# Kernel tuning notes

Hardware: AMD Instinct MI355X
Metric: run time of the kernel (lower is better)

## Reference

```python
import jax, jax.numpy as jnp
from jax import lax
import numpy as np

K, O, I, KS = 4, 128, 128, 5
B, H, W = 32, 64, 64
PAD = 2


def setup_inputs() -> dict:
    key = jax.random.key(0)
    ks = jax.random.split(key, 7)
    x = jax.random.normal(ks[0], (B, I, H, W), dtype=jnp.float32)
    weight = jax.random.normal(ks[1], (K, O, I, KS, KS), dtype=jnp.float32)  # matches torch.randn init
    bias = jax.random.normal(ks[2], (K, O), dtype=jnp.float32)
    # attention: 1x1 convs on a (B,C,1,1) pooled tensor == dense layers
    a1_w = jax.random.normal(ks[3], (I, I), dtype=jnp.float32) * (1.0 / np.sqrt(I))
    a1_b = jax.random.normal(ks[4], (I,), dtype=jnp.float32) * 0.01
    a2_w = jax.random.normal(ks[5], (K, I), dtype=jnp.float32) * (1.0 / np.sqrt(I))
    a2_b = jax.random.normal(ks[6], (K,), dtype=jnp.float32) * 0.01
    return {"x": x, "weight": weight, "bias": bias,
            "a1_w": a1_w, "a1_b": a1_b, "a2_w": a2_w, "a2_b": a2_b}


def reference(x, weight, bias, a1_w, a1_b, a2_w, a2_b):
    Bn = x.shape[0]
    Kn, On, In, kh, kw = weight.shape
    # attention branch: global avg pool -> 1x1 conv -> relu -> 1x1 conv -> softmax over K
    pooled = jnp.mean(x, axis=(2, 3))                       # (B, C)
    h = jax.nn.relu(pooled @ a1_w.T + a1_b)                 # (B, C)
    attn = jax.nn.softmax(h @ a2_w.T + a2_b, axis=1)        # (B, K)
    # K parallel convs fused as one conv with K*O output channels (same math)
    w = weight.reshape(Kn * On, In, kh, kw)
    out = lax.conv_general_dilated(
        x, w, window_strides=(1, 1), padding=((PAD, PAD), (PAD, PAD)),
        dimension_numbers=("NCHW", "OIHW", "NCHW"))        # (B, K*O, H, W)
    Ho, Wo = out.shape[2], out.shape[3]
    out = out.reshape(Bn, Kn, On, Ho, Wo) + bias[None, :, :, None, None]
    # per-sample softmax-weighted combination over the K branches
    return jnp.einsum("bk,bkohw->bohw", attn, out)
```

## Files before the change

### kernel.cpp

```cpp
#include <hip/hip_runtime.h>
#include <stdint.h>

#define BATCH 32
#define ICH 128
#define OCH 128
#define KBR 4
#define HH 64
#define WW 64
#define TAPS 25
#define XROWS 8
#define XCOLS 68
#define XCP 40
#define WROWP 40

typedef __bf16 bf16x8 __attribute__((ext_vector_type(8)));
typedef float f32x4 __attribute__((ext_vector_type(4)));

static __device__ __forceinline__ ushort f2bf(float f) {
    union { float f; uint32_t u; } v; v.f = f;
    uint32_t u = v.u;
    uint32_t r = (u + 0x7FFFu + ((u >> 16) & 1u)) >> 16;
    return (ushort)r;
}
static __device__ __forceinline__ float bf2f(ushort s) {
    union { uint32_t u; float f; } v; v.u = ((uint32_t)s) << 16;
    return v.f;
}

__global__ __launch_bounds__(256) void k_prep(const float* __restrict__ x,
                                              ushort* __restrict__ xT,
                                              float* __restrict__ partial) {
    int blk = blockIdx.x;
    int b = blk >> 6, y = blk & 63;
    __shared__ __align__(16) uint tile2[64][65];
    const float* src = x + ((size_t)b * ICH) * (HH * WW) + (size_t)y * WW;
    int tid = threadIdx.x;
#pragma unroll
    for (int j = 0; j < 4; ++j) {
        int p = tid + 256 * j;
        int i2 = p >> 4, xc = (p & 15) * 4;
        float4 v0 = *(const float4*)(src + (size_t)(2 * i2) * (HH * WW) + xc);
        float4 v1 = *(const float4*)(src + (size_t)(2 * i2 + 1) * (HH * WW) + xc);
        tile2[xc + 0][i2] = (uint)f2bf(v0.x) | ((uint)f2bf(v1.x) << 16);
        tile2[xc + 1][i2] = (uint)f2bf(v0.y) | ((uint)f2bf(v1.y) << 16);
        tile2[xc + 2][i2] = (uint)f2bf(v0.z) | ((uint)f2bf(v1.z) << 16);
        tile2[xc + 3][i2] = (uint)f2bf(v0.w) | ((uint)f2bf(v1.w) << 16);
    }
    __syncthreads();
    uint* dst = (uint*)(xT + (((size_t)b * HH + y) * WW) * ICH);
#pragma unroll
    for (int j = 0; j < 16; ++j) {
        int p2 = tid + 256 * j;
        int xc = p2 >> 6, i2 = p2 & 63;
        dst[p2] = tile2[xc][i2];
    }
    if (tid < 128) {
        int i2 = tid >> 1, half = tid & 1;
        float s = 0.f;
        for (int xc = 0; xc < 64; ++xc) {
            uint v = tile2[xc][i2];
            s += bf2f((ushort)(half ? (v >> 16) : (v & 0xFFFFu)));
        }
        partial[((size_t)b * HH + y) * ICH + tid] = s;
    }
}

__global__ __launch_bounds__(128) void k_attn(const float* __restrict__ partial,
                                              const float* __restrict__ a1_w,
                                              const float* __restrict__ a1_b,
                                              const float* __restrict__ a2_w,
                                              const float* __restrict__ a2_b,
                                              const float* __restrict__ bias,
                                              float* __restrict__ attn,
                                              float* __restrict__ bias_eff) {
    int b = blockIdx.x;
    int t = threadIdx.x;
    __shared__ float pl[128], hh[128], lg[4], at[4];
    {
        float s = 0.f;
        const float* p = partial + (size_t)b * 64 * 128 + t;
        for (int y = 0; y < 64; ++y) s += p[y * 128];
        pl[t] = s * (1.f / 4096.f);
    }
    __syncthreads();
    {
        float a = a1_b[t];
        const float* w1 = a1_w + t * 128;
        for (int i = 0; i < 128; ++i) a += pl[i] * w1[i];
        hh[t] = a > 0.f ? a : 0.f;
    }
    __syncthreads();
    if (t < 4) {
        float l = a2_b[t];
        const float* w2 = a2_w + t * 128;
        for (int i = 0; i < 128; ++i) l += hh[i] * w2[i];
        lg[t] = l;
    }
    __syncthreads();
    if (t == 0) {
        float m = fmaxf(fmaxf(lg[0], lg[1]), fmaxf(lg[2], lg[3]));
        float e0 = expf(lg[0] - m), e1 = expf(lg[1] - m);
        float e2 = expf(lg[2] - m), e3 = expf(lg[3] - m);
        float inv = 1.f / (e0 + e1 + e2 + e3);
        at[0] = e0 * inv; at[1] = e1 * inv; at[2] = e2 * inv; at[3] = e3 * inv;
        attn[b * 4 + 0] = at[0]; attn[b * 4 + 1] = at[1];
        attn[b * 4 + 2] = at[2]; attn[b * 4 + 3] = at[3];
    }
    __syncthreads();
    bias_eff[b * 128 + t] = at[0] * bias[0 * 128 + t] + at[1] * bias[1 * 128 + t] +
                            at[2] * bias[2 * 128 + t] + at[3] * bias[3 * 128 + t];
}

__global__ __launch_bounds__(256) void k_wcomb(const float* __restrict__ weight,
                                               const float* __restrict__ attn,
                                               ushort* __restrict__ Weff) {
    int blk = blockIdx.x;
    int b = blk >> 7, o = blk & 127;
    float a0 = attn[b * 4 + 0], a1 = attn[b * 4 + 1];
    float a2 = attn[b * 4 + 2], a3 = attn[b * 4 + 3];
    __shared__ float wt[3200];
    const float* w = weight + (size_t)o * 3200;
    for (int e = threadIdx.x; e < 3200; e += 256) {
        wt[e] = a0 * w[e] + a1 * w[409600 + e] + a2 * w[819200 + e] + a3 * w[1228800 + e];
    }
    __syncthreads();
    ushort* dst = Weff + ((size_t)(b * 128 + o)) * 3200;
    for (int f = threadIdx.x; f < 3200; f += 256) {
        int t = f >> 7, i = f & 127;
        dst[f] = f2bf(wt[i * 25 + t]);
    }
}

__global__ __launch_bounds__(256, 2) void k_conv(const ushort* __restrict__ xT,
                                                 const ushort* __restrict__ Weff,
                                                 const float* __restrict__ bias_eff,
                                                 float* __restrict__ out) {
    __shared__ __align__(16) ushort lx[XROWS * XCOLS * XCP];
    __shared__ __align__(16) ushort lw[2][128 * WROWP];

    int blk = blockIdx.x;
    int xcd = blk & 7, slot = blk >> 3;
    int b = xcd * 4 + (slot >> 4);
    int rg = slot & 15;
    int y0 = rg * 4;
    int tid = threadIdx.x;
    int lane = tid & 63, wn = tid >> 6;
    int row16 = lane & 15, kg = lane >> 4;

    f32x4 acc[8][4];
    f32x4 zero = {0.f, 0.f, 0.f, 0.f};
#pragma unroll
    for (int m = 0; m < 8; ++m)
#pragma unroll
        for (int n = 0; n < 4; ++n) acc[m][n] = zero;

    const ushort* xb = xT + ((size_t)b * HH * WW) * ICH;
    const ushort* wb = Weff + ((size_t)b * OCH) * 3200;

    int wo0 = tid >> 2, wp0 = tid & 3;
    int wo1 = (tid + 256) >> 2, wp1 = tid & 3;

    {
        for (int q = tid; q < XROWS * XCOLS * 4; q += 256) {
            int s = q / (XCOLS * 4);
            int rem = q - s * (XCOLS * 4);
            int c = rem >> 2, part = rem & 3;
            int gy = y0 - 2 + s, gx = c - 2;
            uint4 val = make_uint4(0u, 0u, 0u, 0u);
            if (gy >= 0 && gy < 64 && gx >= 0 && gx < 64)
                val = *(const uint4*)(xb + ((size_t)(gy * 64 + gx)) * ICH + 0 + part * 8);
            *(uint4*)(&lx[(s * XCOLS + c) * XCP + part * 8]) = val;
        }
        uint4 w0 = *(const uint4*)(wb + ((size_t)wo0 * 25 + 0) * 128 + 0 + wp0 * 8);
        uint4 w1 = *(const uint4*)(wb + ((size_t)wo1 * 25 + 0) * 128 + 0 + wp1 * 8);
        *(uint4*)(&lw[0][wo0 * WROWP + wp0 * 8]) = w0;
        *(uint4*)(&lw[0][wo1 * WROWP + wp1 * 8]) = w1;
    }
    __syncthreads();

    for (int g = 0; g < 100; ++g) {
        int buf = g & 1;
        int t = g % 25;
        uint4 wv0, wv1;
        bool have_next = (g + 1 < 100);
        if (have_next) {
            int gn = g + 1;
            int icn = (gn / 25) * 32, tn = gn % 25;
            wv0 = *(const uint4*)(wb + ((size_t)wo0 * 25 + tn) * 128 + icn + wp0 * 8);
            wv1 = *(const uint4*)(wb + ((size_t)wo1 * 25 + tn) * 128 + icn + wp1 * 8);
        }
        {
            int kh = t / 5, kw = t - kh * 5;
            int s = wn + kh;
            bf16x8 af[8], bfr[4];
#pragma unroll
            for (int n = 0; n < 4; ++n) {
                int cc = n * 16 + row16 + kw;
                bfr[n] = *(const bf16x8*)(&lx[(s * XCOLS + cc) * XCP + kg * 8]);
            }
#pragma unroll
            for (int m = 0; m < 8; ++m) {
                int o = m * 16 + row16;
                af[m] = *(const bf16x8*)(&lw[buf][o * WROWP + kg * 8]);
            }
#pragma unroll
            for (int m = 0; m < 8; ++m)
#pragma unroll
                for (int n = 0; n < 4; ++n)
                    acc[m][n] = __builtin_amdgcn_mfma_f32_16x16x32_bf16(af[m], bfr[n], acc[m][n], 0, 0, 0);
        }
        if (have_next) {
            *(uint4*)(&lw[buf ^ 1][wo0 * WROWP + wp0 * 8]) = wv0;
            *(uint4*)(&lw[buf ^ 1][wo1 * WROWP + wp1 * 8]) = wv1;
        }
        if (t == 24) {
            __syncthreads();
            if (g < 99) {
                int icn = ((g + 1) / 25) * 32;
                for (int q = tid; q < XROWS * XCOLS * 4; q += 256) {
                    int s = q / (XCOLS * 4);
                    int rem = q - s * (XCOLS * 4);
                    int c = rem >> 2, part = rem & 3;
                    int gy = y0 - 2 + s, gx = c - 2;
                    uint4 val = make_uint4(0u, 0u, 0u, 0u);
                    if (gy >= 0 && gy < 64 && gx >= 0 && gx < 64)
                        val = *(const uint4*)(xb + ((size_t)(gy * 64 + gx)) * ICH + icn + part * 8);
                    *(uint4*)(&lx[(s * XCOLS + c) * XCP + part * 8]) = val;
                }
            }
            __syncthreads();
        } else {
            __syncthreads();
        }
    }

    float* ob = out + ((size_t)b * OCH) * (HH * WW);
    int y = y0 + wn;
#pragma unroll
    for (int m = 0; m < 8; ++m) {
#pragma unroll
        for (int r = 0; r < 4; ++r) {
            int o = m * 16 + kg * 4 + r;
            float be = bias_eff[b * 128 + o];
#pragma unroll
            for (int n = 0; n < 4; ++n) {
                int xc = n * 16 + row16;
                ob[((size_t)o * 64 + y) * 64 + xc] = acc[m][n][r] + be;
            }
        }
    }
}

extern "C" void kernel_launch(void* const* d_in, const int* in_sizes, int n_in,
                              void* d_out, int out_size, void* d_ws, size_t ws_size,
                              hipStream_t stream) {
    const float* x      = (const float*)d_in[0];
    const float* weight = (const float*)d_in[1];
    const float* bias   = (const float*)d_in[2];
    const float* a1_w   = (const float*)d_in[3];
    const float* a1_b   = (const float*)d_in[4];
    const float* a2_w   = (const float*)d_in[5];
    const float* a2_b   = (const float*)d_in[6];
    float* out = (float*)d_out;

    const size_t WS_REQUIRED = 60834304;
    if (ws_size < WS_REQUIRED) return;

    char* ws = (char*)d_ws;
    ushort* xT       = (ushort*)(ws);
    ushort* Weff     = (ushort*)(ws + 33554432);
    float*  partial  = (float*)(ws + 59768832);
    float*  attn     = (float*)(ws + 60817408);
    float*  bias_eff = (float*)(ws + 60817920);

    k_prep<<<dim3(BATCH * HH), dim3(256), 0, stream>>>(x, xT, partial);
    k_attn<<<dim3(BATCH), dim3(128), 0, stream>>>(partial, a1_w, a1_b, a2_w, a2_b, bias,
                                                  attn, bias_eff);
    k_wcomb<<<dim3(BATCH * OCH), dim3(256), 0, stream>>>(weight, attn, Weff);
    k_conv<<<dim3(BATCH * 16), dim3(256), 0, stream>>>(xT, Weff, bias_eff, out);
}
```

Measured before the change: 242.6 us.

## Load conv weights directly from global into registers, drop LDS weight staging

Weight fragments are now read from global memory straight into MFMA A-operand registers, double-buffered across two register sets in a loop unrolled by two. The LDS weight buffer and the per-tap __syncthreads are removed; barriers remain only when the input tile is restaged every 25 taps. Each wave now loads its own weight fragments, so global/L2 weight traffic per block rises fourfold and register pressure grows, in exchange for fewer barriers and LDS round trips.

```diff
diff --git a/kernel.cpp b/kernel.cpp
--- a/kernel.cpp
+++ b/kernel.cpp
@@ -11,7 +11,6 @@
 #define XROWS 8
 #define XCOLS 68
 #define XCP 40
-#define WROWP 40
 
 typedef __bf16 bf16x8 __attribute__((ext_vector_type(8)));
 typedef float f32x4 __attribute__((ext_vector_type(4)));
@@ -131,12 +130,37 @@
     }
 }
 
+#define LOADW(af, t, ic)                                                       \
+    {                                                                          \
+        _Pragma("unroll")                                                      \
+        for (int m = 0; m < 8; ++m)                                            \
+            af[m] = *(const bf16x8*)(wlane + m * 51200 + (t) * 128 + (ic));    \
+    }
+
+#define COMPUTE(af, g)                                                         \
+    {                                                                          \
+        int t = (g) % 25;                                                      \
+        int kh = t / 5, kw = t - kh * 5;                                       \
+        int s = wn + kh;                                                       \
+        bf16x8 bfr[4];                                                         \
+        _Pragma("unroll")                                                      \
+        for (int n = 0; n < 4; ++n) {                                          \
+            int cc = n * 16 + row16 + kw;                                      \
+            bfr[n] = *(const bf16x8*)(&lx[(s * XCOLS + cc) * XCP + kg * 8]);   \
+        }                                                                      \
+        _Pragma("unroll")                                                      \
+        for (int m = 0; m < 8; ++m)                                            \
+            _Pragma("unroll")                                                  \
+            for (int n = 0; n < 4; ++n)                                        \
+                acc[m][n] = __builtin_amdgcn_mfma_f32_16x16x32_bf16(           \
+                    af[m], bfr[n], acc[m][n], 0, 0, 0);                        \
+    }
+
 __global__ __launch_bounds__(256, 2) void k_conv(const ushort* __restrict__ xT,
                                                  const ushort* __restrict__ Weff,
                                                  const float* __restrict__ bias_eff,
                                                  float* __restrict__ out) {
     __shared__ __align__(16) ushort lx[XROWS * XCOLS * XCP];
-    __shared__ __align__(16) ushort lw[2][128 * WROWP];
 
     int blk = blockIdx.x;
     int xcd = blk & 7, slot = blk >> 3;
@@ -156,11 +180,9 @@
 
     const ushort* xb = xT + ((size_t)b * HH * WW) * ICH;
     const ushort* wb = Weff + ((size_t)b * OCH) * 3200;
-
-    int wo0 = tid >> 2, wp0 = tid & 3;
-    int wo1 = (tid + 256) >> 2, wp1 = tid & 3;
-
-    {
+    const ushort* wlane = wb + row16 * 3200 + kg * 8;
+
+    auto stage_lx = [&](int ic) {
         for (int q = tid; q < XROWS * XCOLS * 4; q += 256) {
             int s = q / (XCOLS * 4);
             int rem = q - s * (XCOLS * 4);
@@ -168,68 +190,39 @@
             int gy = y0 - 2 + s, gx = c - 2;
             uint4 val = make_uint4(0u, 0u, 0u, 0u);
             if (gy >= 0 && gy < 64 && gx >= 0 && gx < 64)
-                val = *(const uint4*)(xb + ((size_t)(gy * 64 + gx)) * ICH + 0 + part * 8);
+                val = *(const uint4*)(xb + ((size_t)(gy * 64 + gx)) * ICH + ic + part * 8);
             *(uint4*)(&lx[(s * XCOLS + c) * XCP + part * 8]) = val;
         }
-        uint4 w0 = *(const uint4*)(wb + ((size_t)wo0 * 25 + 0) * 128 + 0 + wp0 * 8);
-        uint4 w1 = *(const uint4*)(wb + ((size_t)wo1 * 25 + 0) * 128 + 0 + wp1 * 8);
-        *(uint4*)(&lw[0][wo0 * WROWP + wp0 * 8]) = w0;
-        *(uint4*)(&lw[0][wo1 * WROWP + wp1 * 8]) = w1;
-    }
-    __syncthreads();
-
-    for (int g = 0; g < 100; ++g) {
-        int buf = g & 1;
-        int t = g % 25;
-        uint4 wv0, wv1;
-        bool have_next = (g + 1 < 100);
-        if (have_next) {
-            int gn = g + 1;
-            int icn = (gn / 25) * 32, tn = gn % 25;
-            wv0 = *(const uint4*)(wb + ((size_t)wo0 * 25 + tn) * 128 + icn + wp0 * 8);
-            wv1 = *(const uint4*)(wb + ((size_t)wo1 * 25 + tn) * 128 + icn + wp1 * 8);
-        }
+    };
+
+    stage_lx(0);
+    bf16x8 afA[8], afB[8];
+    LOADW(afA, 0, 0);
+    __syncthreads();
+
+    for (int gp = 0; gp < 50; ++gp) {
+        int g0 = 2 * gp, g1 = g0 + 1;
         {
-            int kh = t / 5, kw = t - kh * 5;
-            int s = wn + kh;
-            bf16x8 af[8], bfr[4];
-#pragma unroll
-            for (int n = 0; n < 4; ++n) {
-                int cc = n * 16 + row16 + kw;
-                bfr[n] = *(const bf16x8*)(&lx[(s * XCOLS + cc) * XCP + kg * 8]);
+            int icn = (g1 / 25) * 32, tn = g1 % 25;
+            LOADW(afB, tn, icn);
+            COMPUTE(afA, g0);
+        }
+        if (g0 % 25 == 24) {
+            __syncthreads();
+            stage_lx(((g0 + 1) / 25) * 32);
+            __syncthreads();
+        }
+        {
+            if (g1 + 1 < 100) {
+                int gn = g1 + 1;
+                int icn = (gn / 25) * 32, tn = gn % 25;
+                LOADW(afA, tn, icn);
             }
-#pragma unroll
-            for (int m = 0; m < 8; ++m) {
-                int o = m * 16 + row16;
-                af[m] = *(const bf16x8*)(&lw[buf][o * WROWP + kg * 8]);
-            }
-#pragma unroll
-            for (int m = 0; m < 8; ++m)
-#pragma unroll
-                for (int n = 0; n < 4; ++n)
-                    acc[m][n] = __builtin_amdgcn_mfma_f32_16x16x32_bf16(af[m], bfr[n], acc[m][n], 0, 0, 0);
-        }
-        if (have_next) {
-            *(uint4*)(&lw[buf ^ 1][wo0 * WROWP + wp0 * 8]) = wv0;
-            *(uint4*)(&lw[buf ^ 1][wo1 * WROWP + wp1 * 8]) = wv1;
-        }
-        if (t == 24) {
-            __syncthreads();
-            if (g < 99) {
-                int icn = ((g + 1) / 25) * 32;
-                for (int q = tid; q < XROWS * XCOLS * 4; q += 256) {
-                    int s = q / (XCOLS * 4);
-                    int rem = q - s * (XCOLS * 4);
-                    int c = rem >> 2, part = rem & 3;
-                    int gy = y0 - 2 + s, gx = c - 2;
-                    uint4 val = make_uint4(0u, 0u, 0u, 0u);
-                    if (gy >= 0 && gy < 64 && gx >= 0 && gx < 64)
-                        val = *(const uint4*)(xb + ((size_t)(gy * 64 + gx)) * ICH + icn + part * 8);
-                    *(uint4*)(&lx[(s * XCOLS + c) * XCP + part * 8]) = val;
-                }
-            }
-            __syncthreads();
-        } else {
+            COMPUTE(afB, g1);
+        }
+        if (g1 % 25 == 24 && g1 < 99) {
+            __syncthreads();
+            stage_lx(((g1 + 1) / 25) * 32);
             __syncthreads();
         }
     }
```

Result: slower. 335.8 us (+38.4%).

## Repack effective weights into MFMA-fragment order for contiguous loads

Applied to the files above, without the earlier changes.

The weight-combine kernel now writes bf16 effective weights in a layout grouped by (tap, input-channel chunk of 8, output channel), so each conv stage's 32-channel by 128-output slab is a contiguous 8 KB block. The conv kernel copies that slab linearly into shared memory and reads A fragments with unpadded, sequential addressing instead of strided per-output rows. This replaces scattered 16-byte global loads with coalesced ones. It drops the row padding that was there to avoid LDS bank conflicts, and the fragment reads could now conflict. The x staging loop is moved into a lambda without changing its behaviour.

```diff
diff --git a/kernel.cpp b/kernel.cpp
--- a/kernel.cpp
+++ b/kernel.cpp
@@ -11,7 +11,6 @@
 #define XROWS 8
 #define XCOLS 68
 #define XCP 40
-#define WROWP 40
 
 typedef __bf16 bf16x8 __attribute__((ext_vector_type(8)));
 typedef float f32x4 __attribute__((ext_vector_type(4)));
@@ -124,10 +123,14 @@
         wt[e] = a0 * w[e] + a1 * w[409600 + e] + a2 * w[819200 + e] + a3 * w[1228800 + e];
     }
     __syncthreads();
-    ushort* dst = Weff + ((size_t)(b * 128 + o)) * 3200;
-    for (int f = threadIdx.x; f < 3200; f += 256) {
-        int t = f >> 7, i = f & 127;
-        dst[f] = f2bf(wt[i * 25 + t]);
+    ushort* dst = Weff + (size_t)b * 409600;
+    for (int f = threadIdx.x; f < 400; f += 256) {
+        int t = f >> 4, c8 = f & 15;
+        uint p0 = (uint)f2bf(wt[(c8 * 8 + 0) * 25 + t]) | ((uint)f2bf(wt[(c8 * 8 + 1) * 25 + t]) << 16);
+        uint p1 = (uint)f2bf(wt[(c8 * 8 + 2) * 25 + t]) | ((uint)f2bf(wt[(c8 * 8 + 3) * 25 + t]) << 16);
+        uint p2 = (uint)f2bf(wt[(c8 * 8 + 4) * 25 + t]) | ((uint)f2bf(wt[(c8 * 8 + 5) * 25 + t]) << 16);
+        uint p3 = (uint)f2bf(wt[(c8 * 8 + 6) * 25 + t]) | ((uint)f2bf(wt[(c8 * 8 + 7) * 25 + t]) << 16);
+        *(uint4*)(&dst[((size_t)(f * 128 + o)) * 8]) = make_uint4(p0, p1, p2, p3);
     }
 }
 
@@ -136,7 +139,7 @@
                                                  const float* __restrict__ bias_eff,
                                                  float* __restrict__ out) {
     __shared__ __align__(16) ushort lx[XROWS * XCOLS * XCP];
-    __shared__ __align__(16) ushort lw[2][128 * WROWP];
+    __shared__ __align__(16) ushort lw[2][4096];
 
     int blk = blockIdx.x;
     int xcd = blk & 7, slot = blk >> 3;
@@ -155,12 +158,9 @@
         for (int n = 0; n < 4; ++n) acc[m][n] = zero;
 
     const ushort* xb = xT + ((size_t)b * HH * WW) * ICH;
-    const ushort* wb = Weff + ((size_t)b * OCH) * 3200;
-
-    int wo0 = tid >> 2, wp0 = tid & 3;
-    int wo1 = (tid + 256) >> 2, wp1 = tid & 3;
-
-    {
+    const ushort* wb2 = Weff + (size_t)b * 409600;
+
+    auto stage_lx = [&](int ic) {
         for (int q = tid; q < XROWS * XCOLS * 4; q += 256) {
             int s = q / (XCOLS * 4);
             int rem = q - s * (XCOLS * 4);
@@ -168,13 +168,15 @@
             int gy = y0 - 2 + s, gx = c - 2;
             uint4 val = make_uint4(0u, 0u, 0u, 0u);
             if (gy >= 0 && gy < 64 && gx >= 0 && gx < 64)
-                val = *(const uint4*)(xb + ((size_t)(gy * 64 + gx)) * ICH + 0 + part * 8);
+                val = *(const uint4*)(xb + ((size_t)(gy * 64 + gx)) * ICH + ic + part * 8);
             *(uint4*)(&lx[(s * XCOLS + c) * XCP + part * 8]) = val;
         }
-        uint4 w0 = *(const uint4*)(wb + ((size_t)wo0 * 25 + 0) * 128 + 0 + wp0 * 8);
-        uint4 w1 = *(const uint4*)(wb + ((size_t)wo1 * 25 + 0) * 128 + 0 + wp1 * 8);
-        *(uint4*)(&lw[0][wo0 * WROWP + wp0 * 8]) = w0;
-        *(uint4*)(&lw[0][wo1 * WROWP + wp1 * 8]) = w1;
+    };
+
+    stage_lx(0);
+    {
+        *(uint4*)(&lw[0][tid * 8])         = *(const uint4*)(wb2 + tid * 8);
+        *(uint4*)(&lw[0][(tid + 256) * 8]) = *(const uint4*)(wb2 + (tid + 256) * 8);
     }
     __syncthreads();
 
@@ -185,9 +187,9 @@
         bool have_next = (g + 1 < 100);
         if (have_next) {
             int gn = g + 1;
-            int icn = (gn / 25) * 32, tn = gn % 25;
-            wv0 = *(const uint4*)(wb + ((size_t)wo0 * 25 + tn) * 128 + icn + wp0 * 8);
-            wv1 = *(const uint4*)(wb + ((size_t)wo1 * 25 + tn) * 128 + icn + wp1 * 8);
+            const ushort* src = wb2 + (size_t)((gn % 25) * 16 + (gn / 25) * 4) * 1024;
+            wv0 = *(const uint4*)(src + tid * 8);
+            wv1 = *(const uint4*)(src + (tid + 256) * 8);
         }
         {
             int kh = t / 5, kw = t - kh * 5;
@@ -200,8 +202,7 @@
             }
 #pragma unroll
             for (int m = 0; m < 8; ++m) {
-                int o = m * 16 + row16;
-                af[m] = *(const bf16x8*)(&lw[buf][o * WROWP + kg * 8]);
+                af[m] = *(const bf16x8*)(&lw[buf][kg * 1024 + m * 128 + row16 * 8]);
             }
 #pragma unroll
             for (int m = 0; m < 8; ++m)
@@ -210,24 +211,12 @@
                     acc[m][n] = __builtin_amdgcn_mfma_f32_16x16x32_bf16(af[m], bfr[n], acc[m][n], 0, 0, 0);
         }
         if (have_next) {
-            *(uint4*)(&lw[buf ^ 1][wo0 * WROWP + wp0 * 8]) = wv0;
-            *(uint4*)(&lw[buf ^ 1][wo1 * WROWP + wp1 * 8]) = wv1;
+            *(uint4*)(&lw[buf ^ 1][tid * 8])         = wv0;
+            *(uint4*)(&lw[buf ^ 1][(tid + 256) * 8]) = wv1;
         }
         if (t == 24) {
             __syncthreads();
-            if (g < 99) {
-                int icn = ((g + 1) / 25) * 32;
-                for (int q = tid; q < XROWS * XCOLS * 4; q += 256) {
-                    int s = q / (XCOLS * 4);
-                    int rem = q - s * (XCOLS * 4);
-                    int c = rem >> 2, part = rem & 3;
-                    int gy = y0 - 2 + s, gx = c - 2;
-                    uint4 val = make_uint4(0u, 0u, 0u, 0u);
-                    if (gy >= 0 && gy < 64 && gx >= 0 && gx < 64)
-                        val = *(const uint4*)(xb + ((size_t)(gy * 64 + gx)) * ICH + icn + part * 8);
-                    *(uint4*)(&lx[(s * XCOLS + c) * XCP + part * 8]) = val;
-                }
-            }
+            if (g < 99) stage_lx(((g + 1) / 25) * 32);
             __syncthreads();
         } else {
             __syncthreads();
```

After: 250.8 us. 1.03x slower.
